# Optimization experiments

Hardware: AMD Instinct MI355X
Metric: run time of the kernel (lower is better)

## Reference

```python
import jax, jax.numpy as jnp
import numpy as np

B, C, IN_LEN, OUT_LEN, E, TOP_K, N_I = 1, 8192, 512, 512, 8, 2, 16


def setup_inputs() -> dict:
    key = jax.random.key(0)
    ks = jax.random.split(key, 8)
    w = lambda k, shape, sc=0.02: jax.random.normal(k, shape, dtype=jnp.float32) * sc
    return {
        "x": jax.random.normal(ks[0], (B, C, IN_LEN), dtype=jnp.float32),
        "Ins_tk": jax.random.normal(ks[1], (B, N_I, OUT_LEN), dtype=jnp.float32),
        "gate_w": w(ks[2], (IN_LEN, E)),            # Gate: Linear(in_len, E, bias=False)
        "expert_w": w(ks[3], (E, IN_LEN, OUT_LEN)),  # per-expert Linear weight (transposed)
        "expert_b": jnp.zeros((E, OUT_LEN), dtype=jnp.float32),
        "gamma_w": w(ks[4], (E, OUT_LEN)),          # EiLM gamma_generator: Linear(h,1,bias=False)
        "beta_w": w(ks[5], (E, OUT_LEN, OUT_LEN)),  # EiLM beta_generator (transposed)
        "rmod_w": w(ks[6], (OUT_LEN, E)),           # router_modulator: Linear(out_len, E, bias=False)
    }


def reference(x, Ins_tk, gate_w, expert_w, expert_b, gamma_w, beta_w, rmod_w):
    Bx, Cx, L = x.shape
    xf = x.reshape(-1, L)                                   # [N, in_len], N = B*C
    ins = Ins_tk[0]                                         # [N_i, out_len] (B==1 asserted)

    # Router: logits + expert-wise modulation of logits
    router_gamma = jnp.mean(ins @ rmod_w, axis=0)           # [E]
    logits = xf @ gate_w + router_gamma                     # [N, E]
    probs = jax.nn.softmax(logits.astype(jnp.float32), axis=-1)
    rw, sel = jax.lax.top_k(probs, TOP_K)                   # [N, k] values/indices (no renorm)

    # Combine weights per token per expert: sum_k rw[t,k] * onehot(sel[t,k])
    combine = jnp.sum(jax.nn.one_hot(sel, E, dtype=rw.dtype) * rw[..., None], axis=1)  # [N, E]

    # EiLM per-expert affine params: scalar gamma, vector beta (mean over instruction tokens)
    gam = jnp.mean(ins @ gamma_w.T, axis=0)                 # [E]
    bet = jnp.einsum('nh,ehd->ed', ins, beta_w) / N_I       # [E, out_len]

    # Per-expert linear over all tokens, then EiLM modulation
    eo = jnp.einsum('nl,eld->end', xf, expert_w) + expert_b[:, None, :]   # [E, N, out]
    mod = gam[:, None, None] * eo + bet[:, None, :]                        # [E, N, out]

    out = jnp.einsum('ne,end->nd', combine, mod)            # [N, out]
    return out.reshape(Bx, Cx, OUT_LEN)
```

## Files before the change

kernel.cpp:

```cpp
#include <hip/hip_runtime.h>
#include <hip/hip_bf16.h>

#define N_TOK 8192
#define INL   512
#define OUTL  512
#define NE    8
#define NI    16
#define EOFF  (OUTL * INL)

typedef unsigned short ushort_t;
typedef unsigned int   uint_t;
typedef short  short8  __attribute__((ext_vector_type(8)));
typedef float  floatx4 __attribute__((ext_vector_type(4)));

#define WS_GAM    2048u
#define WS_RGAM   2080u
#define WS_BET    2112u
#define WS_SELE   18496u
#define WS_SELW   51264u
#define WS_WT     182336u

__device__ __forceinline__ ushort_t f2bf(float f) {
    uint_t b = __float_as_uint(f);
    return (ushort_t)((b + 0x7FFFu + ((b >> 16) & 1u)) >> 16);
}
__device__ __forceinline__ uint_t pkbf(float a, float b) {
    __hip_bfloat162 h = __float22bfloat162_rn(make_float2(a, b));
    union { __hip_bfloat162 h2; uint_t u; } cv;
    cv.h2 = h;
    return cv.u;
}
__device__ __forceinline__ void dma16(const ushort_t* g, ushort_t* l) {
    __builtin_amdgcn_global_load_lds(
        (const __attribute__((address_space(1))) void*)g,
        (__attribute__((address_space(3))) void*)l,
        16, 0, 0);
}

__global__ __launch_bounds__(256)
void k_prep(const float* __restrict__ ins,
            const float* __restrict__ expert_w,
            const float* __restrict__ expert_b,
            const float* __restrict__ gamma_w,
            const float* __restrict__ beta_w,
            const float* __restrict__ rmod_w,
            ushort_t* __restrict__ wt,
            float* __restrict__ wsBet,
            float* __restrict__ wsGam, float* __restrict__ wsRgam) {
    __shared__ __align__(16) char smem[17152];
    int bx = blockIdx.x;
    int tid = threadIdx.x;

    if (bx < 512) {
        float (*tile)[65] = (float(*)[65])smem;
        int e = bx >> 6, rem = bx & 63;
        int lt = (rem >> 3) * 64, dt = (rem & 7) * 64;
        int dIdx = tid & 63, lq = tid >> 6;
        for (int i = 0; i < 16; ++i) {
            int l = lq * 16 + i;
            tile[l][dIdx] = expert_w[(e * INL + lt + l) * OUTL + dt + dIdx];
        }
        __syncthreads();
        int lIdx = tid & 63, dq = tid >> 6;
        for (int i = 0; i < 16; ++i) {
            int d = dq * 16 + i;
            wt[(e * OUTL + dt + d) * INL + lt + lIdx] = f2bf(tile[lIdx][d]);
        }
        return;
    }

    if (bx < 640) {
        float* sS  = (float*)smem;
        float* red = sS + 512;
        float* gamS = red + 256;
        int b2 = bx - 512;
        int e = b2 >> 4, dBase = (b2 & 15) * 32;
        for (int h = tid; h < INL; h += 256) {
            float a = 0.f;
            for (int n = 0; n < NI; ++n) a += ins[n * INL + h];
            sS[h] = a;
        }
        __syncthreads();
        if (tid < 64) {
            float g = 0.f;
            for (int j = 0; j < 8; ++j) g += sS[tid * 8 + j] * gamma_w[e * INL + tid * 8 + j];
            for (int off = 32; off >= 1; off >>= 1) g += __shfl_xor(g, off, 64);
            if (tid == 0) gamS[0] = g * (1.f / NI);
        }
        int doff = tid & 31, hq = tid >> 5;
        float a = 0.f;
        for (int j = 0; j < 64; ++j) {
            int h = hq * 64 + j;
            a += sS[h] * beta_w[(e * INL + h) * OUTL + dBase + doff];
        }
        red[tid] = a;
        __syncthreads();
        if (tid < 32) {
            float t = 0.f;
            for (int k = 0; k < 8; ++k) t += red[k * 32 + tid];
            int d = dBase + tid;
            wsBet[e * OUTL + d] = t * (1.f / NI) + gamS[0] * expert_b[e * OUTL + d];
        }
        return;
    }

    {
        float* sS = (float*)smem;
        float* pg = sS + 512;
        float* pr = pg + 64;
        for (int h = tid; h < INL; h += 256) {
            float a = 0.f;
            for (int n = 0; n < NI; ++n) a += ins[n * INL + h];
            sS[h] = a;
        }
        __syncthreads();
        if (tid < 64) {
            int e = tid & 7, qq = tid >> 3;
            float g = 0.f, r = 0.f;
            for (int j = 0; j < 64; ++j) {
                int h = qq * 64 + j;
                float sv = sS[h];
                g += sv * gamma_w[e * INL + h];
                r += sv * rmod_w[h * NE + e];
            }
            pg[tid] = g; pr[tid] = r;
        }
        __syncthreads();
        if (tid < NE) {
            float g = 0.f, r = 0.f;
            for (int qq = 0; qq < 8; ++qq) { g += pg[qq * 8 + tid]; r += pr[qq * 8 + tid]; }
            wsGam[tid]  = g * (1.f / NI);
            wsRgam[tid] = r * (1.f / NI);
        }
    }
}

__global__ void k_route(const float* __restrict__ x,
                        const float* __restrict__ gate_w,
                        const float* __restrict__ wsGam,
                        const float* __restrict__ wsRgam,
                        int* __restrict__ selE, float4* __restrict__ selW) {
    __shared__ float gateT[NE * INL];
    int tid = threadIdx.x;
    for (int i = 0; i < 16; ++i) {
        int f = tid + 256 * i;
        float v = gate_w[f];
        gateT[(f & 7) * INL + (f >> 3)] = v;
    }
    __syncthreads();

    int w = tid >> 6, lane = tid & 63;
    int tbase = blockIdx.x * 16 + w * 4;

    for (int tt = 0; tt < 4; ++tt) {
        int t = tbase + tt;
        float2 xv[4];
        for (int i = 0; i < 4; ++i)
            xv[i] = *(const float2*)(x + (size_t)t * INL + 2 * lane + 128 * i);

        float acc[NE];
        for (int e = 0; e < NE; ++e) acc[e] = 0.f;
        for (int i = 0; i < 4; ++i) {
            int c = 2 * lane + 128 * i;
            for (int e = 0; e < NE; ++e)
                acc[e] += xv[i].x * gateT[e * INL + c] + xv[i].y * gateT[e * INL + c + 1];
        }
        for (int e = 0; e < NE; ++e) {
            float a = acc[e];
            for (int off = 32; off >= 1; off >>= 1) a += __shfl_xor(a, off, 64);
            acc[e] = a;
        }
        float logit[NE];
        for (int e = 0; e < NE; ++e) logit[e] = acc[e] + wsRgam[e];

        int i0 = 0; float m0 = logit[0];
        for (int e = 1; e < NE; ++e) if (logit[e] > m0) { m0 = logit[e]; i0 = e; }
        int i1 = -1; float m1 = -3.4e38f;
        for (int e = 0; e < NE; ++e) if (e != i0 && logit[e] > m1) { m1 = logit[e]; i1 = e; }

        float S = 0.f;
        for (int e = 0; e < NE; ++e) S += expf(logit[e] - m0);
        float rw0 = 1.0f / S;
        float rw1 = expf(m1 - m0) / S;

        if (lane == 0) {
            selE[t] = i0 | (i1 << 8);
            selW[t] = make_float4(rw0 * wsGam[i0], rw1 * wsGam[i1], rw0, rw1);
        }
    }
}

__global__ __launch_bounds__(256, 4)
void k_gemm(const float* __restrict__ x, const ushort_t* __restrict__ wt,
            const int* __restrict__ selE, const float4* __restrict__ selW,
            const float* __restrict__ wsBet, float* __restrict__ out) {
    int bx = blockIdx.x;
    int rt = bx & 127;
    int ct = bx >> 7;
    __shared__ ushort_t Blds[2][64 * 64];

    int tid = threadIdx.x;
    int wid = tid >> 6, lane = tid & 63;
    int wm = wid * 16;
    int mrow = lane & 15, laneq = lane >> 4, q8 = laneq * 8, qr = laneq * 4;

    int tokL = rt * 64 + wm + mrow;
    float wv[NE];
    {
        int es = selE[tokL];
        float4 w4 = selW[tokL];
        int e0 = es & 255, e1 = es >> 8;
        for (int e = 0; e < NE; ++e)
            wv[e] = (e == e0) ? w4.x : ((e == e1) ? w4.y : 0.f);
    }
    const float* arowp = x + (size_t)tokL * INL + q8;

    int c0 = tid, c1 = tid + 256;
    int col0 = c0 >> 3, kg0 = ((c0 & 7) - col0) & 7;
    int col1 = c1 >> 3, kg1 = ((c1 & 7) - col1) & 7;
    const ushort_t* pB0 = wt + (size_t)(ct * 64 + col0) * INL + kg0 * 8;
    const ushort_t* pB1 = wt + (size_t)(ct * 64 + col1) * INL + kg1 * 8;
    ushort_t* ldsW0 = &Blds[0][0] + (wid * 64) * 8;
    ushort_t* ldsW1 = &Blds[0][0] + (256 + wid * 64) * 8;

    int fcol[4], frot0[4];
    for (int nt = 0; nt < 4; ++nt) {
        fcol[nt] = nt * 16 + mrow;
        frot0[nt] = (laneq + fcol[nt]) & 7;
    }

    floatx4 comb[4];
    for (int nt = 0; nt < 4; ++nt) comb[nt] = (floatx4){0.f, 0.f, 0.f, 0.f};

    dma16(pB0, ldsW0);
    dma16(pB1, ldsW1);
    __syncthreads();

    float4 ar[2][2];

    #pragma unroll 1
    for (int kc = 0; kc < 8; ++kc) {
        for (int ks = 0; ks < 2; ++ks) {
            const float* p = arowp + kc * 64 + ks * 32;
            ar[ks][0] = *(const float4*)p;
            ar[ks][1] = *(const float4*)(p + 4);
        }

        #pragma unroll
        for (int e = 0; e < NE; ++e) {
            int step = kc * 8 + e;
            int buf = step & 1;
            int ne = e + 1, nkc = kc;
            if (ne == NE) { ne = 0; nkc = kc + 1; }
            if (nkc < 8) {
                size_t off = (size_t)ne * EOFF + (size_t)nkc * 64;
                int nb = (step + 1) & 1;
                dma16(pB0 + off, ldsW0 + nb * 4096);
                dma16(pB1 + off, ldsW1 + nb * 4096);
            }

            const ushort_t* B = &Blds[buf][0];
            short8 bf[4][2];
            for (int nt = 0; nt < 4; ++nt) {
                int cb = fcol[nt] * 64;
                bf[nt][0] = *(const short8*)&B[cb + frot0[nt] * 8];
                bf[nt][1] = *(const short8*)&B[cb + ((frot0[nt] + 4) & 7) * 8];
            }
            float w = wv[e];
            for (int ks = 0; ks < 2; ++ks) {
                union { uint4 u; short8 s; } af;
                float4 a0 = ar[ks][0], a1 = ar[ks][1];
                af.u.x = pkbf(a0.x * w, a0.y * w);
                af.u.y = pkbf(a0.z * w, a0.w * w);
                af.u.z = pkbf(a1.x * w, a1.y * w);
                af.u.w = pkbf(a1.z * w, a1.w * w);
                for (int nt = 0; nt < 4; ++nt)
                    comb[nt] = __builtin_amdgcn_mfma_f32_16x16x32_bf16(
                        af.s, bf[nt][ks], comb[nt], 0, 0, 0);
            }
            __syncthreads();
        }
    }

    for (int ri = 0; ri < 4; ++ri) {
        int row = wm + qr + ri;
        int tok = rt * 64 + row;
        int es = selE[tok];
        float4 w4 = selW[tok];
        int e0 = es & 255, e1 = es >> 8;
        for (int nt = 0; nt < 4; ++nt) {
            int col = ct * 64 + nt * 16 + mrow;
            float bet = w4.z * wsBet[e0 * OUTL + col] + w4.w * wsBet[e1 * OUTL + col];
            out[(size_t)tok * OUTL + col] = comb[nt][ri] + bet;
        }
    }
}

extern "C" void kernel_launch(void* const* d_in, const int* in_sizes, int n_in,
                              void* d_out, int out_size, void* d_ws, size_t ws_size,
                              hipStream_t stream) {
    const float* x        = (const float*)d_in[0];
    const float* ins      = (const float*)d_in[1];
    const float* gate_w   = (const float*)d_in[2];
    const float* expert_w = (const float*)d_in[3];
    const float* expert_b = (const float*)d_in[4];
    const float* gamma_w  = (const float*)d_in[5];
    const float* beta_w   = (const float*)d_in[6];
    const float* rmod_w   = (const float*)d_in[7];
    float* out = (float*)d_out;

    char* ws = (char*)d_ws;
    float*    wsGam  = (float*)(ws + WS_GAM);
    float*    wsRgam = (float*)(ws + WS_RGAM);
    float*    wsBet  = (float*)(ws + WS_BET);
    int*      selE   = (int*)(ws + WS_SELE);
    float4*   selW   = (float4*)(ws + WS_SELW);
    ushort_t* wt     = (ushort_t*)(ws + WS_WT);

    k_prep<<<641, 256, 0, stream>>>(ins, expert_w, expert_b,
                                    gamma_w, beta_w, rmod_w,
                                    wt, wsBet, wsGam, wsRgam);
    k_route<<<N_TOK / 16, 256, 0, stream>>>(x, gate_w, wsGam, wsRgam, selE, selW);
    k_gemm<<<1024, 256, 0, stream>>>(x, wt, selE, selW, wsBet, out);
}
```

Measured before the change: 154.5 us.

## Replace dense all-expert GEMM with sparse grouped GEMM over routed token lists

Result: slower. 183.6 us (+18.9%).

```diff
diff --git a/kernel.cpp b/kernel.cpp
--- a/kernel.cpp
+++ b/kernel.cpp
@@ -13,12 +13,15 @@
 typedef short  short8  __attribute__((ext_vector_type(8)));
 typedef float  floatx4 __attribute__((ext_vector_type(4)));
 
+#define WS_CNT    0u
 #define WS_GAM    2048u
 #define WS_RGAM   2080u
 #define WS_BET    2112u
 #define WS_SELE   18496u
 #define WS_SELW   51264u
 #define WS_WT     182336u
+#define WS_LIST   4380672u
+#define MAXT      136
 
 __device__ __forceinline__ ushort_t f2bf(float f) {
     uint_t b = __float_as_uint(f);
@@ -46,7 +49,8 @@
             const float* __restrict__ rmod_w,
             ushort_t* __restrict__ wt,
             float* __restrict__ wsBet,
-            float* __restrict__ wsGam, float* __restrict__ wsRgam) {
+            float* __restrict__ wsGam, float* __restrict__ wsRgam,
+            int* __restrict__ wsCnt) {
     __shared__ __align__(16) char smem[17152];
     int bx = blockIdx.x;
     int tid = threadIdx.x;
@@ -105,6 +109,7 @@
     }
 
     {
+        if (tid < 16) wsCnt[tid * 16] = 0;
         float* sS = (float*)smem;
         float* pg = sS + 512;
         float* pr = pg + 64;
@@ -139,7 +144,8 @@
                         const float* __restrict__ gate_w,
                         const float* __restrict__ wsGam,
                         const float* __restrict__ wsRgam,
-                        int* __restrict__ selE, float4* __restrict__ selW) {
+                        int* __restrict__ selE, float4* __restrict__ selW,
+                        int* __restrict__ wsCnt, int* __restrict__ wsList) {
     __shared__ float gateT[NE * INL];
     int tid = threadIdx.x;
     for (int i = 0; i < 16; ++i) {
@@ -186,17 +192,35 @@
         if (lane == 0) {
             selE[t] = i0 | (i1 << 8);
             selW[t] = make_float4(rw0 * wsGam[i0], rw1 * wsGam[i1], rw0, rw1);
-        }
-    }
-}
-
+            int p0 = atomicAdd(wsCnt + i0 * 16, 1);
+            wsList[i0 * N_TOK + p0] = t;
+            int p1 = atomicAdd(wsCnt + (8 + i1) * 16, 1);
+            wsList[(8 + i1) * N_TOK + p1] = t;
+        }
+    }
+}
+
+template<int PASS>
 __global__ __launch_bounds__(256, 4)
-void k_gemm(const float* __restrict__ x, const ushort_t* __restrict__ wt,
-            const int* __restrict__ selE, const float4* __restrict__ selW,
-            const float* __restrict__ wsBet, float* __restrict__ out) {
+void k_gemm2(const float* __restrict__ x, const ushort_t* __restrict__ wt,
+             const int* __restrict__ wsCnt, const int* __restrict__ wsList,
+             const int* __restrict__ selE, const float4* __restrict__ selW,
+             const float* __restrict__ wsBet, float* __restrict__ out) {
     int bx = blockIdx.x;
-    int rt = bx & 127;
-    int ct = bx >> 7;
+    int ct = bx & 7;
+    int bt = bx >> 3;
+
+    int e = -1, lt = 0, cntE = 0, run = 0;
+    #pragma unroll
+    for (int i = 0; i < 8; ++i) {
+        int ci = wsCnt[(PASS * 8 + i) * 16];
+        int ti = (ci + 63) >> 6;
+        if (e < 0 && bt < run + ti) { e = i; lt = bt - run; cntE = ci; }
+        run += ti;
+    }
+    if (e < 0) return;
+    const int* listE = wsList + (PASS * 8 + e) * N_TOK;
+
     __shared__ ushort_t Blds[2][64 * 64];
 
     int tid = threadIdx.x;
@@ -204,22 +228,20 @@
     int wm = wid * 16;
     int mrow = lane & 15, laneq = lane >> 4, q8 = laneq * 8, qr = laneq * 4;
 
-    int tokL = rt * 64 + wm + mrow;
-    float wv[NE];
-    {
-        int es = selE[tokL];
-        float4 w4 = selW[tokL];
-        int e0 = es & 255, e1 = es >> 8;
-        for (int e = 0; e < NE; ++e)
-            wv[e] = (e == e0) ? w4.x : ((e == e1) ? w4.y : 0.f);
-    }
-    const float* arowp = x + (size_t)tokL * INL + q8;
+    int idx = lt * 64 + wm + mrow;
+    int tok = 0; float w = 0.f;
+    if (idx < cntE) {
+        tok = listE[idx];
+        float4 w4 = selW[tok];
+        w = PASS ? w4.y : w4.x;
+    }
+    const float* arowp = x + (size_t)tok * INL + q8;
 
     int c0 = tid, c1 = tid + 256;
     int col0 = c0 >> 3, kg0 = ((c0 & 7) - col0) & 7;
     int col1 = c1 >> 3, kg1 = ((c1 & 7) - col1) & 7;
-    const ushort_t* pB0 = wt + (size_t)(ct * 64 + col0) * INL + kg0 * 8;
-    const ushort_t* pB1 = wt + (size_t)(ct * 64 + col1) * INL + kg1 * 8;
+    const ushort_t* pB0 = wt + (size_t)e * EOFF + (size_t)(ct * 64 + col0) * INL + kg0 * 8;
+    const ushort_t* pB1 = wt + (size_t)e * EOFF + (size_t)(ct * 64 + col1) * INL + kg1 * 8;
     ushort_t* ldsW0 = &Blds[0][0] + (wid * 64) * 8;
     ushort_t* ldsW1 = &Blds[0][0] + (256 + wid * 64) * 8;
 
@@ -246,52 +268,54 @@
             ar[ks][1] = *(const float4*)(p + 4);
         }
 
-        #pragma unroll
-        for (int e = 0; e < NE; ++e) {
-            int step = kc * 8 + e;
-            int buf = step & 1;
-            int ne = e + 1, nkc = kc;
-            if (ne == NE) { ne = 0; nkc = kc + 1; }
-            if (nkc < 8) {
-                size_t off = (size_t)ne * EOFF + (size_t)nkc * 64;
-                int nb = (step + 1) & 1;
-                dma16(pB0 + off, ldsW0 + nb * 4096);
-                dma16(pB1 + off, ldsW1 + nb * 4096);
-            }
-
-            const ushort_t* B = &Blds[buf][0];
-            short8 bf[4][2];
-            for (int nt = 0; nt < 4; ++nt) {
-                int cb = fcol[nt] * 64;
-                bf[nt][0] = *(const short8*)&B[cb + frot0[nt] * 8];
-                bf[nt][1] = *(const short8*)&B[cb + ((frot0[nt] + 4) & 7) * 8];
-            }
-            float w = wv[e];
-            for (int ks = 0; ks < 2; ++ks) {
-                union { uint4 u; short8 s; } af;
-                float4 a0 = ar[ks][0], a1 = ar[ks][1];
-                af.u.x = pkbf(a0.x * w, a0.y * w);
-                af.u.y = pkbf(a0.z * w, a0.w * w);
-                af.u.z = pkbf(a1.x * w, a1.y * w);
-                af.u.w = pkbf(a1.z * w, a1.w * w);
-                for (int nt = 0; nt < 4; ++nt)
-                    comb[nt] = __builtin_amdgcn_mfma_f32_16x16x32_bf16(
-                        af.s, bf[nt][ks], comb[nt], 0, 0, 0);
-            }
-            __syncthreads();
-        }
+        int buf = kc & 1;
+        if (kc < 7) {
+            size_t off = (size_t)(kc + 1) * 64;
+            int nb = buf ^ 1;
+            dma16(pB0 + off, ldsW0 + nb * 4096);
+            dma16(pB1 + off, ldsW1 + nb * 4096);
+        }
+
+        const ushort_t* B = &Blds[buf][0];
+        short8 bf[4][2];
+        for (int nt = 0; nt < 4; ++nt) {
+            int cb = fcol[nt] * 64;
+            bf[nt][0] = *(const short8*)&B[cb + frot0[nt] * 8];
+            bf[nt][1] = *(const short8*)&B[cb + ((frot0[nt] + 4) & 7) * 8];
+        }
+        for (int ks = 0; ks < 2; ++ks) {
+            union { uint4 u; short8 s; } af;
+            float4 a0 = ar[ks][0], a1 = ar[ks][1];
+            af.u.x = pkbf(a0.x * w, a0.y * w);
+            af.u.y = pkbf(a0.z * w, a0.w * w);
+            af.u.z = pkbf(a1.x * w, a1.y * w);
+            af.u.w = pkbf(a1.z * w, a1.w * w);
+            for (int nt = 0; nt < 4; ++nt)
+                comb[nt] = __builtin_amdgcn_mfma_f32_16x16x32_bf16(
+                    af.s, bf[nt][ks], comb[nt], 0, 0, 0);
+        }
+        __syncthreads();
     }
 
     for (int ri = 0; ri < 4; ++ri) {
         int row = wm + qr + ri;
-        int tok = rt * 64 + row;
-        int es = selE[tok];
-        float4 w4 = selW[tok];
-        int e0 = es & 255, e1 = es >> 8;
-        for (int nt = 0; nt < 4; ++nt) {
-            int col = ct * 64 + nt * 16 + mrow;
-            float bet = w4.z * wsBet[e0 * OUTL + col] + w4.w * wsBet[e1 * OUTL + col];
-            out[(size_t)tok * OUTL + col] = comb[nt][ri] + bet;
+        int idx2 = lt * 64 + row;
+        if (idx2 >= cntE) continue;
+        int tok2 = listE[idx2];
+        if (PASS == 0) {
+            int es = selE[tok2];
+            float4 w4 = selW[tok2];
+            int e0 = es & 255, e1 = es >> 8;
+            for (int nt = 0; nt < 4; ++nt) {
+                int col = ct * 64 + nt * 16 + mrow;
+                float bet = w4.z * wsBet[e0 * OUTL + col] + w4.w * wsBet[e1 * OUTL + col];
+                out[(size_t)tok2 * OUTL + col] = comb[nt][ri] + bet;
+            }
+        } else {
+            for (int nt = 0; nt < 4; ++nt) {
+                int col = ct * 64 + nt * 16 + mrow;
+                out[(size_t)tok2 * OUTL + col] += comb[nt][ri];
+            }
         }
     }
 }
@@ -310,16 +334,22 @@
     float* out = (float*)d_out;
 
     char* ws = (char*)d_ws;
+    int*      wsCnt  = (int*)(ws + WS_CNT);
     float*    wsGam  = (float*)(ws + WS_GAM);
     float*    wsRgam = (float*)(ws + WS_RGAM);
     float*    wsBet  = (float*)(ws + WS_BET);
     int*      selE   = (int*)(ws + WS_SELE);
     float4*   selW   = (float4*)(ws + WS_SELW);
     ushort_t* wt     = (ushort_t*)(ws + WS_WT);
+    int*      wsList = (int*)(ws + WS_LIST);
 
     k_prep<<<641, 256, 0, stream>>>(ins, expert_w, expert_b,
                                     gamma_w, beta_w, rmod_w,
-                                    wt, wsBet, wsGam, wsRgam);
-    k_route<<<N_TOK / 16, 256, 0, stream>>>(x, gate_w, wsGam, wsRgam, selE, selW);
-    k_gemm<<<1024, 256, 0, stream>>>(x, wt, selE, selW, wsBet, out);
-}
+                                    wt, wsBet, wsGam, wsRgam, wsCnt);
+    k_route<<<N_TOK / 16, 256, 0, stream>>>(x, gate_w, wsGam, wsRgam,
+                                            selE, selW, wsCnt, wsList);
+    k_gemm2<0><<<MAXT * 8, 256, 0, stream>>>(x, wt, wsCnt, wsList,
+                                             selE, selW, wsBet, out);
+    k_gemm2<1><<<MAXT * 8, 256, 0, stream>>>(x, wt, wsCnt, wsList,
+                                             selE, selW, wsBet, out);
+}
```
